# Kernel tuning notes

Measured on AMD Instinct MI355X. Metric: run time of the kernel, lower is better.

## Reference

```python
import jax, jax.numpy as jnp
import numpy as np

N = 256      # n_nodes (complete graph -> E = N*N edges)
HID = 128    # hid_dim
L = 4        # num_layers
NCAT = 64    # number of edge-orbit categories
CIN, COUT = 2, 3
B = 8
E = N * N


def _ln(x, g, b, eps=1e-5):
    m = x.mean(-1, keepdims=True)
    v = ((x - m) ** 2).mean(-1, keepdims=True)
    return (x - m) * jax.lax.rsqrt(v + eps) * g + b


def _mlp(x, W1, b1, g1, bt1, W2, b2, g2, bt2):
    # Linear -> LayerNorm -> ReLU -> Linear -> LayerNorm
    h = jax.nn.relu(_ln(x @ W1 + b1, g1, bt1))
    return _ln(h @ W2 + b2, g2, bt2)


def setup_inputs() -> dict:
    key = jax.random.key(0)
    ks = jax.random.split(key, 10)
    s = 0.05
    ii = jnp.arange(N, dtype=jnp.int32)
    edge_src = jnp.repeat(ii, N)   # i of (i,j), matches [(i,j) for i for j]
    edge_dst = jnp.tile(ii, N)     # j of (i,j)
    edge_cat = jax.random.randint(ks[0], (E,), 0, NCAT, dtype=jnp.int32)
    return dict(
        x=jax.random.normal(ks[1], (B, N, CIN), jnp.float32),
        emb=jax.random.normal(ks[2], (NCAT, HID), jnp.float32),
        in_W1=jax.random.normal(ks[3], (CIN, HID), jnp.float32) * s,
        in_b1=jnp.zeros(HID), in_g1=jnp.ones(HID), in_bt1=jnp.zeros(HID),
        in_W2=jax.random.normal(ks[4], (HID, HID), jnp.float32) * s,
        in_b2=jnp.zeros(HID), in_g2=jnp.ones(HID), in_bt2=jnp.zeros(HID),
        conv_W1=jax.random.normal(ks[5], (L, HID, HID), jnp.float32) * s,
        conv_b1=jnp.zeros((L, HID)), conv_g1=jnp.ones((L, HID)), conv_bt1=jnp.zeros((L, HID)),
        conv_W2=jax.random.normal(ks[6], (L, HID, HID), jnp.float32) * s,
        conv_b2=jnp.zeros((L, HID)), conv_g2=jnp.ones((L, HID)), conv_bt2=jnp.zeros((L, HID)),
        conv_eps=jnp.zeros(L),
        ln_g=jnp.ones((L, HID)), ln_b=jnp.zeros((L, HID)),
        out_W=jax.random.normal(ks[7], (HID, COUT), jnp.float32) * s,
        out_b=jnp.zeros(COUT),
        edge_src=edge_src, edge_dst=edge_dst, edge_cat=edge_cat,
    )


def reference(x, emb, in_W1, in_b1, in_g1, in_bt1, in_W2, in_b2, in_g2, in_bt2,
              conv_W1, conv_b1, conv_g1, conv_bt1, conv_W2, conv_b2, conv_g2, conv_bt2,
              conv_eps, ln_g, ln_b, out_W, out_b, edge_src, edge_dst, edge_cat):
    # EdgeEmbedder: per-category max-norm clip (all norms = 1.0 in the dense path)
    e = emb[edge_cat]                                  # [E, HID]
    cn = jnp.linalg.norm(e, axis=1, keepdims=True)
    cn = jnp.where(cn == 0, 1e-8, cn)
    e = e * jnp.minimum(1.0, 1.0 / cn)

    def item(xi):                                      # xi: [N, CIN]
        h = _mlp(xi, in_W1, in_b1, in_g1, in_bt1, in_W2, in_b2, in_g2, in_bt2)
        for l in range(L):
            # GINEConv: msg = relu(x_j + e_ij), aggregate (sum) at destination
            msg = jax.nn.relu(h[edge_src] + e)          # [E, HID]
            agg = jax.ops.segment_sum(msg, edge_dst, num_segments=N)
            h2 = _mlp((1.0 + conv_eps[l]) * h + agg,
                      conv_W1[l], conv_b1[l], conv_g1[l], conv_bt1[l],
                      conv_W2[l], conv_b2[l], conv_g2[l], conv_bt2[l])
            h = jax.nn.relu(_ln(h2, ln_g[l], ln_b[l])) + h
        return h @ out_W + out_b                        # [N, COUT]

    return jax.vmap(item)(x)                            # [B, N, COUT]
```

## Files before the change

kernel.cpp:

```cpp
#include <hip/hip_runtime.h>

#define HID 128
#define NN  256
#define BB  8
#define NCATS 64

__device__ inline void ln_stats(float a, float c, float& mean, float& rs) {
    float s = a + c;
    float q = a * a + c * c;
    #pragma unroll
    for (int m = 32; m; m >>= 1) {
        s += __shfl_xor(s, m);
        q += __shfl_xor(q, m);
    }
    mean = s * (1.0f / 128.0f);
    float var = q * (1.0f / 128.0f) - mean * mean;
    rs = rsqrtf(var + 1e-5f);
}

__global__ __launch_bounds__(512) void k_setup(
    const float* __restrict__ x, const float* __restrict__ emb,
    const float* __restrict__ inW1, const float* __restrict__ inb1,
    const float* __restrict__ ing1, const float* __restrict__ inbt1,
    const float* __restrict__ inW2, const float* __restrict__ inb2,
    const float* __restrict__ ing2, const float* __restrict__ inbt2,
    const int* __restrict__ ecat,
    float* __restrict__ ne, uint2* __restrict__ catp, float* __restrict__ h0)
{
    __shared__ __align__(16) float sV[8][128];
    __shared__ __align__(16) float sH1[8][128];
    __shared__ __align__(16) float sA[4][8][128];

    const int blk = blockIdx.x;
    const int t = threadIdx.x;
    const int w = t >> 6, lane = t & 63;

    if (blk < 256) {
        const int row0 = blk * 8;
        for (int item = t; item < 1024; item += 512) {
            int r = item >> 7, dd = item & 127;
            int row = row0 + r;
            float x0 = x[row * 2 + 0], x1 = x[row * 2 + 1];
            sV[r][dd] = fmaf(x0, inW1[dd], fmaf(x1, inW1[128 + dd], inb1[dd]));
        }
        __syncthreads();
        {
            float a = sV[w][lane], c = sV[w][lane + 64];
            float mean, rs; ln_stats(a, c, mean, rs);
            sH1[w][lane]      = fmaxf((a - mean) * rs * ing1[lane]      + inbt1[lane],      0.f);
            sH1[w][lane + 64] = fmaxf((c - mean) * rs * ing1[lane + 64] + inbt1[lane + 64], 0.f);
        }
        __syncthreads();
        {
            int dd = t & 127, ks = t >> 7;
            float acc[8] = {0.f, 0.f, 0.f, 0.f, 0.f, 0.f, 0.f, 0.f};
            for (int k = ks * 32; k < ks * 32 + 32; ++k) {
                float wv = inW2[k * 128 + dd];
                #pragma unroll
                for (int r = 0; r < 8; ++r) acc[r] = fmaf(sH1[r][k], wv, acc[r]);
            }
            #pragma unroll
            for (int r = 0; r < 8; ++r) sA[ks][r][dd] = acc[r];
        }
        __syncthreads();
        for (int item = t; item < 1024; item += 512) {
            int r = item >> 7, dd = item & 127;
            sV[r][dd] = inb2[dd] + sA[0][r][dd] + sA[1][r][dd] + sA[2][r][dd] + sA[3][r][dd];
        }
        __syncthreads();
        {
            float a = sV[w][lane], c = sV[w][lane + 64];
            float mean, rs; ln_stats(a, c, mean, rs);
            int row = row0 + w;
            h0[row * HID + lane]      = (a - mean) * rs * ing2[lane]      + inbt2[lane];
            h0[row * HID + lane + 64] = (c - mean) * rs * ing2[lane + 64] + inbt2[lane + 64];
        }
    } else if (blk < 264) {
        int r = (blk - 256) * 8 + w;
        float a = emb[r * 128 + lane], c = emb[r * 128 + lane + 64];
        float q = a * a + c * c;
        #pragma unroll
        for (int m = 32; m; m >>= 1) q += __shfl_xor(q, m);
        float cn = sqrtf(q);
        if (cn == 0.f) cn = 1e-8f;
        float sc = fminf(1.0f, 1.0f / cn);
        ne[r * 128 + lane]      = a * sc;
        ne[r * 128 + lane + 64] = c * sc;
    } else {
        int jb = blk - 264;
        if (t < 256) {
            int i = t;
            const int* p = ecat + i * NN + jb * 8;
            int4 c0 = *(const int4*)p;
            int4 c1 = *(const int4*)(p + 4);
            unsigned lo = (unsigned)c0.x | ((unsigned)c0.y << 8) |
                          ((unsigned)c0.z << 16) | ((unsigned)c0.w << 24);
            unsigned hi = (unsigned)c1.x | ((unsigned)c1.y << 8) |
                          ((unsigned)c1.z << 16) | ((unsigned)c1.w << 24);
            catp[jb * 256 + i] = make_uint2(lo, hi);
        }
    }
}

__global__ __launch_bounds__(512) void k_layer(
    const float* __restrict__ h_old, float* __restrict__ h_new,
    const float* __restrict__ ne, const uint2* __restrict__ catp,
    const float* __restrict__ W1, const float* __restrict__ b1,
    const float* __restrict__ g1, const float* __restrict__ bt1,
    const float* __restrict__ W2, const float* __restrict__ b2,
    const float* __restrict__ g2, const float* __restrict__ bt2,
    const float* __restrict__ epsp,
    const float* __restrict__ lng, const float* __restrict__ lnb,
    const float* __restrict__ outW, const float* __restrict__ outb,
    float* __restrict__ dout, int isLast)
{
    __shared__ __align__(16) float sNe[NCATS * HID];
    __shared__ __align__(16) float sAcc[16 * 8 * 128];
    __shared__ __align__(16) uint2 sCat[256];
    __shared__ __align__(16) float sU[8][128];
    __shared__ __align__(16) float sH1[8][128];
    __shared__ __align__(16) float sV[8][128];

    const int t = threadIdx.x;
    const int b = blockIdx.x >> 5;
    const int jb = blockIdx.x & 31;
    const int w = t >> 6, lane = t & 63;
    const float* hb = h_old + (size_t)b * NN * HID;

    for (int idx = t; idx < NCATS * HID / 4; idx += 512)
        ((float4*)sNe)[idx] = ((const float4*)ne)[idx];
    if (t < 256) sCat[t] = catp[jb * 256 + t];
    __syncthreads();

    const int dg = t & 31;
    const int ig = t >> 5;
    float4 acc[8];
    #pragma unroll
    for (int k = 0; k < 8; ++k) acc[k] = make_float4(0.f, 0.f, 0.f, 0.f);

    for (int n = 0; n < 16; ++n) {
        int i = ig * 16 + n;
        float4 hv = *(const float4*)(hb + i * HID + dg * 4);
        uint2 c8 = sCat[i];
        #pragma unroll
        for (int k = 0; k < 8; ++k) {
            unsigned c = ((k < 4 ? (c8.x >> (8 * k)) : (c8.y >> (8 * (k - 4)))) & 255u);
            float4 nv = *(const float4*)&sNe[c * HID + dg * 4];
            acc[k].x += fmaxf(hv.x + nv.x, 0.f);
            acc[k].y += fmaxf(hv.y + nv.y, 0.f);
            acc[k].z += fmaxf(hv.z + nv.z, 0.f);
            acc[k].w += fmaxf(hv.w + nv.w, 0.f);
        }
    }
    #pragma unroll
    for (int k = 0; k < 8; ++k)
        *(float4*)&sAcc[(ig * 8 + k) * 128 + dg * 4] = acc[k];
    __syncthreads();

    const float eps1 = 1.0f + epsp[0];
    for (int item = t; item < 1024; item += 512) {
        int r = item >> 7, dd = item & 127;
        float s = 0.f;
        #pragma unroll
        for (int igx = 0; igx < 16; ++igx) s += sAcc[(igx * 8 + r) * 128 + dd];
        sU[r][dd] = eps1 * hb[(jb * 8 + r) * HID + dd] + s;
    }
    __syncthreads();

    {
        int dd = t & 127, ks = t >> 7;
        float a8[8] = {0.f, 0.f, 0.f, 0.f, 0.f, 0.f, 0.f, 0.f};
        for (int k = ks * 32; k < ks * 32 + 32; ++k) {
            float wv = W1[k * 128 + dd];
            #pragma unroll
            for (int r = 0; r < 8; ++r) a8[r] = fmaf(sU[r][k], wv, a8[r]);
        }
        #pragma unroll
        for (int r = 0; r < 8; ++r) sAcc[(ks * 8 + r) * 128 + dd] = a8[r];
    }
    __syncthreads();
    for (int item = t; item < 1024; item += 512) {
        int r = item >> 7, dd = item & 127;
        sV[r][dd] = b1[dd] + sAcc[r * 128 + dd] + sAcc[(8 + r) * 128 + dd] +
                    sAcc[(16 + r) * 128 + dd] + sAcc[(24 + r) * 128 + dd];
    }
    __syncthreads();

    {
        float a = sV[w][lane], c = sV[w][lane + 64];
        float mean, rs; ln_stats(a, c, mean, rs);
        sH1[w][lane]      = fmaxf((a - mean) * rs * g1[lane]      + bt1[lane],      0.f);
        sH1[w][lane + 64] = fmaxf((c - mean) * rs * g1[lane + 64] + bt1[lane + 64], 0.f);
    }
    __syncthreads();

    {
        int dd = t & 127, ks = t >> 7;
        float a8[8] = {0.f, 0.f, 0.f, 0.f, 0.f, 0.f, 0.f, 0.f};
        for (int k = ks * 32; k < ks * 32 + 32; ++k) {
            float wv = W2[k * 128 + dd];
            #pragma unroll
            for (int r = 0; r < 8; ++r) a8[r] = fmaf(sH1[r][k], wv, a8[r]);
        }
        #pragma unroll
        for (int r = 0; r < 8; ++r) sAcc[(ks * 8 + r) * 128 + dd] = a8[r];
    }
    __syncthreads();
    for (int item = t; item < 1024; item += 512) {
        int r = item >> 7, dd = item & 127;
        sV[r][dd] = b2[dd] + sAcc[r * 128 + dd] + sAcc[(8 + r) * 128 + dd] +
                    sAcc[(16 + r) * 128 + dd] + sAcc[(24 + r) * 128 + dd];
    }
    __syncthreads();

    {
        float a = sV[w][lane], c = sV[w][lane + 64];
        float mean, rs; ln_stats(a, c, mean, rs);
        float y1 = (a - mean) * rs * g2[lane]      + bt2[lane];
        float y2 = (c - mean) * rs * g2[lane + 64] + bt2[lane + 64];

        float mean3, rs3; ln_stats(y1, y2, mean3, rs3);
        int row = jb * 8 + w;
        int grow = b * NN + row;
        float ho1 = hb[row * HID + lane], ho2 = hb[row * HID + lane + 64];
        float z1 = fmaxf((y1 - mean3) * rs3 * lng[lane]      + lnb[lane],      0.f) + ho1;
        float z2 = fmaxf((y2 - mean3) * rs3 * lng[lane + 64] + lnb[lane + 64], 0.f) + ho2;

        if (!isLast) {
            h_new[(size_t)grow * HID + lane]      = z1;
            h_new[(size_t)grow * HID + lane + 64] = z2;
        } else {
            #pragma unroll
            for (int cc = 0; cc < 3; ++cc) {
                float p = z1 * outW[lane * 3 + cc] + z2 * outW[(lane + 64) * 3 + cc];
                #pragma unroll
                for (int m = 32; m; m >>= 1) p += __shfl_xor(p, m);
                if (lane == 0) dout[grow * 3 + cc] = p + outb[cc];
            }
        }
    }
}

extern "C" void kernel_launch(void* const* d_in, const int* in_sizes, int n_in,
                              void* d_out, int out_size, void* d_ws, size_t ws_size,
                              hipStream_t stream) {
    const float* x     = (const float*)d_in[0];
    const float* emb   = (const float*)d_in[1];
    const float* inW1  = (const float*)d_in[2];
    const float* inb1  = (const float*)d_in[3];
    const float* ing1  = (const float*)d_in[4];
    const float* inbt1 = (const float*)d_in[5];
    const float* inW2  = (const float*)d_in[6];
    const float* inb2  = (const float*)d_in[7];
    const float* ing2  = (const float*)d_in[8];
    const float* inbt2 = (const float*)d_in[9];
    const float* cW1   = (const float*)d_in[10];
    const float* cb1   = (const float*)d_in[11];
    const float* cg1   = (const float*)d_in[12];
    const float* cbt1  = (const float*)d_in[13];
    const float* cW2   = (const float*)d_in[14];
    const float* cb2   = (const float*)d_in[15];
    const float* cg2   = (const float*)d_in[16];
    const float* cbt2  = (const float*)d_in[17];
    const float* ceps  = (const float*)d_in[18];
    const float* lng   = (const float*)d_in[19];
    const float* lnb   = (const float*)d_in[20];
    const float* outW  = (const float*)d_in[21];
    const float* outb  = (const float*)d_in[22];
    const int*   ecat  = (const int*)d_in[25];

    float* ws   = (float*)d_ws;
    float* ne   = ws;
    uint2* catp = (uint2*)(ws + 8192);
    float* hA   = ws + 8192 + 16384;
    float* hB   = hA + BB * NN * HID;
    float* out  = (float*)d_out;

    k_setup<<<296, 512, 0, stream>>>(x, emb, inW1, inb1, ing1, inbt1,
                                     inW2, inb2, ing2, inbt2, ecat, ne, catp, hA);

    for (int l = 0; l < 4; ++l) {
        const float* ho = (l & 1) ? hB : hA;
        float*       hn = (l & 1) ? hA : hB;
        k_layer<<<256, 512, 0, stream>>>(
            ho, hn, ne, catp,
            cW1 + l * HID * HID, cb1 + l * HID, cg1 + l * HID, cbt1 + l * HID,
            cW2 + l * HID * HID, cb2 + l * HID, cg2 + l * HID, cbt2 + l * HID,
            ceps + l, lng + l * HID, lnb + l * HID,
            outW, outb, out, (l == 3) ? 1 : 0);
    }
}
```

Measured before the change: 74.44 us.

## Store edge embeddings and MLP activations as bf16, preload weights into registers

Edge-category embeddings are packed to bf16, which halves the shared-memory footprint and LDS traffic in the message-aggregation loop. The per-row h vectors are preloaded into registers before the loop. The MLP weight columns are prefetched into registers before the barriers. The MLP inputs are packed into transposed bf16 tiles so the GEMV reads one uint4 per k. This trades numerical precision (bf16 rounding of embeddings and activations) and higher register pressure, which may lower occupancy, for less memory traffic and latency.

```diff
diff --git a/kernel.cpp b/kernel.cpp
--- a/kernel.cpp
+++ b/kernel.cpp
@@ -4,6 +4,16 @@
 #define NN  256
 #define BB  8
 #define NCATS 64
+
+__device__ inline unsigned pack_bf16(float lo, float hi) {
+    unsigned ul = __float_as_uint(lo);
+    unsigned uh = __float_as_uint(hi);
+    ul = (ul + 0x7fffu + ((ul >> 16) & 1u)) >> 16;
+    uh = (uh + 0x7fffu + ((uh >> 16) & 1u)) & 0xffff0000u;
+    return ul | uh;
+}
+__device__ inline float bf_lo(unsigned v) { return __uint_as_float(v << 16); }
+__device__ inline float bf_hi(unsigned v) { return __uint_as_float(v & 0xffff0000u); }
 
 __device__ inline void ln_stats(float a, float c, float& mean, float& rs) {
     float s = a + c;
@@ -25,23 +35,29 @@
     const float* __restrict__ inW2, const float* __restrict__ inb2,
     const float* __restrict__ ing2, const float* __restrict__ inbt2,
     const int* __restrict__ ecat,
-    float* __restrict__ ne, uint2* __restrict__ catp, float* __restrict__ h0)
+    unsigned* __restrict__ nep, uint2* __restrict__ catp, float* __restrict__ h0)
 {
     __shared__ __align__(16) float sV[8][128];
     __shared__ __align__(16) float sH1[8][128];
     __shared__ __align__(16) float sA[4][8][128];
+    __shared__ __align__(16) uint4 sH1T[128];
 
     const int blk = blockIdx.x;
     const int t = threadIdx.x;
     const int w = t >> 6, lane = t & 63;
 
     if (blk < 256) {
+        const int dd = t & 127, ks = t >> 7;
+        float w2r[32];
+        #pragma unroll
+        for (int k = 0; k < 32; ++k) w2r[k] = inW2[(ks * 32 + k) * 128 + dd];
+
         const int row0 = blk * 8;
         for (int item = t; item < 1024; item += 512) {
-            int r = item >> 7, dd = item & 127;
+            int r = item >> 7, d2 = item & 127;
             int row = row0 + r;
             float x0 = x[row * 2 + 0], x1 = x[row * 2 + 1];
-            sV[r][dd] = fmaf(x0, inW1[dd], fmaf(x1, inW1[128 + dd], inb1[dd]));
+            sV[r][d2] = fmaf(x0, inW1[d2], fmaf(x1, inW1[128 + d2], inb1[d2]));
         }
         __syncthreads();
         {
@@ -52,20 +68,32 @@
         }
         __syncthreads();
         {
-            int dd = t & 127, ks = t >> 7;
-            float acc[8] = {0.f, 0.f, 0.f, 0.f, 0.f, 0.f, 0.f, 0.f};
-            for (int k = ks * 32; k < ks * 32 + 32; ++k) {
-                float wv = inW2[k * 128 + dd];
-                #pragma unroll
-                for (int r = 0; r < 8; ++r) acc[r] = fmaf(sH1[r][k], wv, acc[r]);
+            int kd = t & 127, wr = t >> 7;
+            ((unsigned*)sH1T)[kd * 4 + wr] = pack_bf16(sH1[2 * wr][kd], sH1[2 * wr + 1][kd]);
+        }
+        __syncthreads();
+        {
+            float a8[8] = {0.f,0.f,0.f,0.f,0.f,0.f,0.f,0.f};
+            #pragma unroll
+            for (int k = 0; k < 32; ++k) {
+                uint4 a = sH1T[ks * 32 + k];
+                float wv = w2r[k];
+                a8[0] = fmaf(bf_lo(a.x), wv, a8[0]);
+                a8[1] = fmaf(bf_hi(a.x), wv, a8[1]);
+                a8[2] = fmaf(bf_lo(a.y), wv, a8[2]);
+                a8[3] = fmaf(bf_hi(a.y), wv, a8[3]);
+                a8[4] = fmaf(bf_lo(a.z), wv, a8[4]);
+                a8[5] = fmaf(bf_hi(a.z), wv, a8[5]);
+                a8[6] = fmaf(bf_lo(a.w), wv, a8[6]);
+                a8[7] = fmaf(bf_hi(a.w), wv, a8[7]);
             }
             #pragma unroll
-            for (int r = 0; r < 8; ++r) sA[ks][r][dd] = acc[r];
+            for (int r = 0; r < 8; ++r) sA[ks][r][dd] = a8[r];
         }
         __syncthreads();
         for (int item = t; item < 1024; item += 512) {
-            int r = item >> 7, dd = item & 127;
-            sV[r][dd] = inb2[dd] + sA[0][r][dd] + sA[1][r][dd] + sA[2][r][dd] + sA[3][r][dd];
+            int r = item >> 7, d2 = item & 127;
+            sV[r][d2] = inb2[d2] + sA[0][r][d2] + sA[1][r][d2] + sA[2][r][d2] + sA[3][r][d2];
         }
         __syncthreads();
         {
@@ -77,15 +105,14 @@
         }
     } else if (blk < 264) {
         int r = (blk - 256) * 8 + w;
-        float a = emb[r * 128 + lane], c = emb[r * 128 + lane + 64];
-        float q = a * a + c * c;
+        float2 em = *(const float2*)(emb + r * 128 + 2 * lane);
+        float q = em.x * em.x + em.y * em.y;
         #pragma unroll
         for (int m = 32; m; m >>= 1) q += __shfl_xor(q, m);
         float cn = sqrtf(q);
         if (cn == 0.f) cn = 1e-8f;
         float sc = fminf(1.0f, 1.0f / cn);
-        ne[r * 128 + lane]      = a * sc;
-        ne[r * 128 + lane + 64] = c * sc;
+        nep[r * 64 + lane] = pack_bf16(em.x * sc, em.y * sc);
     } else {
         int jb = blk - 264;
         if (t < 256) {
@@ -104,7 +131,7 @@
 
 __global__ __launch_bounds__(512) void k_layer(
     const float* __restrict__ h_old, float* __restrict__ h_new,
-    const float* __restrict__ ne, const uint2* __restrict__ catp,
+    const uint4* __restrict__ nep4, const uint2* __restrict__ catp,
     const float* __restrict__ W1, const float* __restrict__ b1,
     const float* __restrict__ g1, const float* __restrict__ bt1,
     const float* __restrict__ W2, const float* __restrict__ b2,
@@ -114,11 +141,12 @@
     const float* __restrict__ outW, const float* __restrict__ outb,
     float* __restrict__ dout, int isLast)
 {
-    __shared__ __align__(16) float sNe[NCATS * HID];
-    __shared__ __align__(16) float sAcc[16 * 8 * 128];
+    __shared__ __align__(16) uint4 sNe4[NCATS * 16];
+    __shared__ __align__(16) float sPart[16 * 8 * 128];
     __shared__ __align__(16) uint2 sCat[256];
-    __shared__ __align__(16) float sU[8][128];
+    __shared__ __align__(16) uint4 sUT[128];
     __shared__ __align__(16) float sH1[8][128];
+    __shared__ __align__(16) uint4 sH1T[128];
     __shared__ __align__(16) float sV[8][128];
 
     const int t = threadIdx.x;
@@ -126,63 +154,89 @@
     const int jb = blockIdx.x & 31;
     const int w = t >> 6, lane = t & 63;
     const float* hb = h_old + (size_t)b * NN * HID;
-
-    for (int idx = t; idx < NCATS * HID / 4; idx += 512)
-        ((float4*)sNe)[idx] = ((const float4*)ne)[idx];
+    const uint2* sNe2 = (const uint2*)sNe4;
+
+    for (int idx = t; idx < 1024; idx += 512) sNe4[idx] = nep4[idx];
     if (t < 256) sCat[t] = catp[jb * 256 + t];
     __syncthreads();
 
     const int dg = t & 31;
     const int ig = t >> 5;
-    float4 acc[8];
-    #pragma unroll
-    for (int k = 0; k < 8; ++k) acc[k] = make_float4(0.f, 0.f, 0.f, 0.f);
-
+    float4 hv[16];
+    #pragma unroll
+    for (int n = 0; n < 16; ++n)
+        hv[n] = *(const float4*)(hb + (ig * 16 + n) * HID + dg * 4);
+
+    float acc[8][4];
+    #pragma unroll
+    for (int k = 0; k < 8; ++k)
+        #pragma unroll
+        for (int d = 0; d < 4; ++d) acc[k][d] = 0.f;
+
+    #pragma unroll
     for (int n = 0; n < 16; ++n) {
-        int i = ig * 16 + n;
-        float4 hv = *(const float4*)(hb + i * HID + dg * 4);
-        uint2 c8 = sCat[i];
+        uint2 c8 = sCat[ig * 16 + n];
+        float hx = hv[n].x, hy = hv[n].y, hz = hv[n].z, hw = hv[n].w;
         #pragma unroll
         for (int k = 0; k < 8; ++k) {
             unsigned c = ((k < 4 ? (c8.x >> (8 * k)) : (c8.y >> (8 * (k - 4)))) & 255u);
-            float4 nv = *(const float4*)&sNe[c * HID + dg * 4];
-            acc[k].x += fmaxf(hv.x + nv.x, 0.f);
-            acc[k].y += fmaxf(hv.y + nv.y, 0.f);
-            acc[k].z += fmaxf(hv.z + nv.z, 0.f);
-            acc[k].w += fmaxf(hv.w + nv.w, 0.f);
+            uint2 nv = sNe2[c * 32 + dg];
+            acc[k][0] += fmaxf(hx + bf_lo(nv.x), 0.f);
+            acc[k][1] += fmaxf(hy + bf_hi(nv.x), 0.f);
+            acc[k][2] += fmaxf(hz + bf_lo(nv.y), 0.f);
+            acc[k][3] += fmaxf(hw + bf_hi(nv.y), 0.f);
         }
     }
     #pragma unroll
     for (int k = 0; k < 8; ++k)
-        *(float4*)&sAcc[(ig * 8 + k) * 128 + dg * 4] = acc[k];
-    __syncthreads();
-
-    const float eps1 = 1.0f + epsp[0];
+        *(float4*)&sPart[(ig * 8 + k) * 128 + dg * 4] =
+            make_float4(acc[k][0], acc[k][1], acc[k][2], acc[k][3]);
+
+    const int dd = t & 127, ks = t >> 7;
+    float w1r[32], w2r[32];
+    #pragma unroll
+    for (int k = 0; k < 32; ++k) w1r[k] = W1[(ks * 32 + k) * 128 + dd];
+    #pragma unroll
+    for (int k = 0; k < 32; ++k) w2r[k] = W2[(ks * 32 + k) * 128 + dd];
+    __syncthreads();
+
+    {
+        const int kd = t & 127, wr = t >> 7;
+        const float eps1 = 1.0f + epsp[0];
+        float u0 = eps1 * hb[(jb * 8 + 2 * wr) * HID + kd];
+        float u1 = eps1 * hb[(jb * 8 + 2 * wr + 1) * HID + kd];
+        #pragma unroll
+        for (int g = 0; g < 16; ++g) {
+            u0 += sPart[(g * 8 + 2 * wr) * 128 + kd];
+            u1 += sPart[(g * 8 + 2 * wr + 1) * 128 + kd];
+        }
+        ((unsigned*)sUT)[kd * 4 + wr] = pack_bf16(u0, u1);
+    }
+    __syncthreads();
+
+    {
+        float a8[8] = {0.f,0.f,0.f,0.f,0.f,0.f,0.f,0.f};
+        #pragma unroll
+        for (int k = 0; k < 32; ++k) {
+            uint4 a = sUT[ks * 32 + k];
+            float wv = w1r[k];
+            a8[0] = fmaf(bf_lo(a.x), wv, a8[0]);
+            a8[1] = fmaf(bf_hi(a.x), wv, a8[1]);
+            a8[2] = fmaf(bf_lo(a.y), wv, a8[2]);
+            a8[3] = fmaf(bf_hi(a.y), wv, a8[3]);
+            a8[4] = fmaf(bf_lo(a.z), wv, a8[4]);
+            a8[5] = fmaf(bf_hi(a.z), wv, a8[5]);
+            a8[6] = fmaf(bf_lo(a.w), wv, a8[6]);
+            a8[7] = fmaf(bf_hi(a.w), wv, a8[7]);
+        }
+        #pragma unroll
+        for (int r = 0; r < 8; ++r) sPart[(ks * 8 + r) * 128 + dd] = a8[r];
+    }
+    __syncthreads();
     for (int item = t; item < 1024; item += 512) {
-        int r = item >> 7, dd = item & 127;
-        float s = 0.f;
-        #pragma unroll
-        for (int igx = 0; igx < 16; ++igx) s += sAcc[(igx * 8 + r) * 128 + dd];
-        sU[r][dd] = eps1 * hb[(jb * 8 + r) * HID + dd] + s;
-    }
-    __syncthreads();
-
-    {
-        int dd = t & 127, ks = t >> 7;
-        float a8[8] = {0.f, 0.f, 0.f, 0.f, 0.f, 0.f, 0.f, 0.f};
-        for (int k = ks * 32; k < ks * 32 + 32; ++k) {
-            float wv = W1[k * 128 + dd];
-            #pragma unroll
-            for (int r = 0; r < 8; ++r) a8[r] = fmaf(sU[r][k], wv, a8[r]);
-        }
-        #pragma unroll
-        for (int r = 0; r < 8; ++r) sAcc[(ks * 8 + r) * 128 + dd] = a8[r];
-    }
-    __syncthreads();
-    for (int item = t; item < 1024; item += 512) {
-        int r = item >> 7, dd = item & 127;
-        sV[r][dd] = b1[dd] + sAcc[r * 128 + dd] + sAcc[(8 + r) * 128 + dd] +
-                    sAcc[(16 + r) * 128 + dd] + sAcc[(24 + r) * 128 + dd];
+        int r = item >> 7, d2 = item & 127;
+        sV[r][d2] = b1[d2] + sPart[r * 128 + d2] + sPart[(8 + r) * 128 + d2] +
+                    sPart[(16 + r) * 128 + d2] + sPart[(24 + r) * 128 + d2];
     }
     __syncthreads();
 
@@ -193,23 +247,35 @@
         sH1[w][lane + 64] = fmaxf((c - mean) * rs * g1[lane + 64] + bt1[lane + 64], 0.f);
     }
     __syncthreads();
-
-    {
-        int dd = t & 127, ks = t >> 7;
-        float a8[8] = {0.f, 0.f, 0.f, 0.f, 0.f, 0.f, 0.f, 0.f};
-        for (int k = ks * 32; k < ks * 32 + 32; ++k) {
-            float wv = W2[k * 128 + dd];
-            #pragma unroll
-            for (int r = 0; r < 8; ++r) a8[r] = fmaf(sH1[r][k], wv, a8[r]);
-        }
-        #pragma unroll
-        for (int r = 0; r < 8; ++r) sAcc[(ks * 8 + r) * 128 + dd] = a8[r];
+    {
+        const int kd = t & 127, wr = t >> 7;
+        ((unsigned*)sH1T)[kd * 4 + wr] = pack_bf16(sH1[2 * wr][kd], sH1[2 * wr + 1][kd]);
+    }
+    __syncthreads();
+
+    {
+        float a8[8] = {0.f,0.f,0.f,0.f,0.f,0.f,0.f,0.f};
+        #pragma unroll
+        for (int k = 0; k < 32; ++k) {
+            uint4 a = sH1T[ks * 32 + k];
+            float wv = w2r[k];
+            a8[0] = fmaf(bf_lo(a.x), wv, a8[0]);
+            a8[1] = fmaf(bf_hi(a.x), wv, a8[1]);
+            a8[2] = fmaf(bf_lo(a.y), wv, a8[2]);
+            a8[3] = fmaf(bf_hi(a.y), wv, a8[3]);
+            a8[4] = fmaf(bf_lo(a.z), wv, a8[4]);
+            a8[5] = fmaf(bf_hi(a.z), wv, a8[5]);
+            a8[6] = fmaf(bf_lo(a.w), wv, a8[6]);
+            a8[7] = fmaf(bf_hi(a.w), wv, a8[7]);
+        }
+        #pragma unroll
+        for (int r = 0; r < 8; ++r) sPart[(ks * 8 + r) * 128 + dd] = a8[r];
     }
     __syncthreads();
     for (int item = t; item < 1024; item += 512) {
-        int r = item >> 7, dd = item & 127;
-        sV[r][dd] = b2[dd] + sAcc[r * 128 + dd] + sAcc[(8 + r) * 128 + dd] +
-                    sAcc[(16 + r) * 128 + dd] + sAcc[(24 + r) * 128 + dd];
+        int r = item >> 7, d2 = item & 127;
+        sV[r][d2] = b2[d2] + sPart[r * 128 + d2] + sPart[(8 + r) * 128 + d2] +
+                    sPart[(16 + r) * 128 + d2] + sPart[(24 + r) * 128 + d2];
     }
     __syncthreads();
 
@@ -270,20 +336,20 @@
     const int*   ecat  = (const int*)d_in[25];
 
     float* ws   = (float*)d_ws;
-    float* ne   = ws;
-    uint2* catp = (uint2*)(ws + 8192);
-    float* hA   = ws + 8192 + 16384;
+    unsigned* nep = (unsigned*)ws;
+    uint2* catp = (uint2*)(ws + 4096);
+    float* hA   = ws + 4096 + 16384;
     float* hB   = hA + BB * NN * HID;
     float* out  = (float*)d_out;
 
     k_setup<<<296, 512, 0, stream>>>(x, emb, inW1, inb1, ing1, inbt1,
-                                     inW2, inb2, ing2, inbt2, ecat, ne, catp, hA);
+                                     inW2, inb2, ing2, inbt2, ecat, nep, catp, hA);
 
     for (int l = 0; l < 4; ++l) {
         const float* ho = (l & 1) ? hB : hA;
         float*       hn = (l & 1) ? hA : hB;
         k_layer<<<256, 512, 0, stream>>>(
-            ho, hn, ne, catp,
+            ho, hn, (const uint4*)nep, catp,
             cW1 + l * HID * HID, cb1 + l * HID, cg1 + l * HID, cbt1 + l * HID,
             cW2 + l * HID * HID, cb2 + l * HID, cg2 + l * HID, cbt2 + l * HID,
             ceps + l, lng + l * HID, lnb + l * HID,
```

Measured after the change: 166.0 us. 2.23x slower.
